# Performance work log

Measured on AMD Instinct MI355X. Metric: run time of the kernel, lower is better.

Reference implementation:

```python
import jax, jax.numpy as jnp
import numpy as np

SINKHORN_ITERS = 4
EPS = 1e-6


def setup_inputs() -> dict:
    key = jax.random.key(0)
    B, T, W, D = 2, 4096, 4, 2048
    k1, k2 = jax.random.split(key, 2)
    x = jax.random.normal(k1, (B, T, W, D), dtype=jnp.float32)
    W_router = jax.random.normal(k2, (W * W + 2 * W, D), dtype=jnp.float32) * 0.02
    b_router = jnp.zeros((W * W + 2 * W,), dtype=jnp.float32)
    return {"x": x, "W_router": W_router, "b_router": b_router}


def _sinkhorn(logits):
    # Bistochastic projection: 4 iterations of alternating row/col normalization.
    def body(w, _):
        w = w / jnp.maximum(w.sum(axis=-1, keepdims=True), EPS)
        w = w / jnp.maximum(w.sum(axis=-2, keepdims=True), EPS)
        return w, None
    w, _ = jax.lax.scan(body, jnp.exp(logits), None, length=SINKHORN_ITERS)
    return w


def reference(x, W_router, b_router):
    B, T, W, D = x.shape
    # router input: mean over the width (stream) dim -> (B, T, D)
    routing_input = x.mean(axis=2)
    raw = routing_input @ W_router.T + b_router          # (B, T, W*W + 2W)
    pre = jax.nn.softmax(raw[..., :W], axis=-1)          # (B, T, W)
    post = jax.nn.softmax(raw[..., W:2 * W], axis=-1)    # (B, T, W)
    res_logits = raw[..., 2 * W:].reshape(B, T, W, W)
    # residual_bias buffer: -2 off-diagonal, +2 on diagonal
    idx = jnp.arange(W)
    bias = jnp.full((W, W), -2.0, dtype=x.dtype).at[idx, idx].set(2.0)
    residual = _sinkhorn(res_logits + bias)              # (B, T, W, W)
    # aggregate streams with pre weights, apply op (identity here)
    aggregated = (x * pre[..., None]).sum(axis=2)        # (B, T, D)
    op_out = aggregated                                  # op = identity
    mixed_residual = jnp.einsum('btij,btjd->btid', residual, x)
    return mixed_residual + post[..., None] * op_out[:, :, None, :]
```

## Files before the change

kernel.cpp:

```cpp
#include <hip/hip_runtime.h>


#define SINKHORN_ITERS 4
#define EPSV 1e-6f

typedef float f32x4 __attribute__((ext_vector_type(4)));

__global__ __launch_bounds__(256, 4) void mchc_fused(
    const float* __restrict__ x,
    const float* __restrict__ Wr,
    const float* __restrict__ br,
    float* __restrict__ out)
{
    const int token = blockIdx.x;
    const int tid   = threadIdx.x;
    const int lane  = tid & 63;
    const int wave  = tid >> 6;

    const f32x4* __restrict__ x4 = (const f32x4*)(x + (size_t)token * 8192);
    const f32x4* __restrict__ w4 = (const f32x4*)Wr;
    f32x4*       __restrict__ o4 = (f32x4*)(out + (size_t)token * 8192);

    f32x4 xa[4], xb[4];
#pragma unroll
    for (int w = 0; w < 4; ++w) {
        xa[w] = __builtin_nontemporal_load(&x4[w * 512 + tid]);
        xb[w] = __builtin_nontemporal_load(&x4[w * 512 + 256 + tid]);
    }

    f32x4 sa = xa[0] + xa[1] + xa[2] + xa[3];
    f32x4 sb = xb[0] + xb[1] + xb[2] + xb[3];

    float p[24];
#pragma unroll
    for (int g = 0; g < 3; ++g) {
        f32x4 wa[8], wb[8];
#pragma unroll
        for (int r = 0; r < 8; ++r) {
            wa[r] = w4[(g * 8 + r) * 512 + tid];
            wb[r] = w4[(g * 8 + r) * 512 + 256 + tid];
        }
        __builtin_amdgcn_sched_barrier(0);
#pragma unroll
        for (int r = 0; r < 8; ++r) {
            f32x4 t = sa * wa[r] + sb * wb[r];
            p[g * 8 + r] = t.x + t.y + t.z + t.w;
        }
    }

    __shared__ float red[4][24];
    __shared__ float rawbuf[24];
    __shared__ float Mbuf[16];

#pragma unroll
    for (int k = 0; k < 24; ++k) {
        float v = p[k];
        v += __shfl_xor(v, 1);
        v += __shfl_xor(v, 2);
        v += __shfl_xor(v, 4);
        v += __shfl_xor(v, 8);
        v += __shfl_xor(v, 16);
        v += __shfl_xor(v, 32);
        p[k] = v;
    }
    if (lane == 0) {
#pragma unroll
        for (int k = 0; k < 24; ++k) red[wave][k] = p[k];
    }
    __syncthreads();

    if (tid < 24) {
        float r = red[0][tid] + red[1][tid] + red[2][tid] + red[3][tid];
        rawbuf[tid] = 0.25f * r + br[tid];
    }
    __syncthreads();

    if (tid < 16) {
        const int i = tid >> 2, j = tid & 3;

        float r0 = rawbuf[0], r1 = rawbuf[1], r2 = rawbuf[2], r3 = rawbuf[3];
        float mp = fmaxf(fmaxf(r0, r1), fmaxf(r2, r3));
        float sp = __expf(r0 - mp) + __expf(r1 - mp) + __expf(r2 - mp) + __expf(r3 - mp);
        float pre_j = __expf(rawbuf[j] - mp) / sp;

        float q0 = rawbuf[4], q1 = rawbuf[5], q2 = rawbuf[6], q3 = rawbuf[7];
        float mq = fmaxf(fmaxf(q0, q1), fmaxf(q2, q3));
        float sq = __expf(q0 - mq) + __expf(q1 - mq) + __expf(q2 - mq) + __expf(q3 - mq);
        float post_i = __expf(rawbuf[4 + i] - mq) / sq;

        float w = __expf(rawbuf[8 + tid] + ((i == j) ? 2.0f : -2.0f));
#pragma unroll
        for (int it = 0; it < SINKHORN_ITERS; ++it) {
            float rs = w + __shfl_xor(w, 1);
            rs += __shfl_xor(rs, 2);
            w /= fmaxf(rs, EPSV);
            float cs = w + __shfl_xor(w, 4);
            cs += __shfl_xor(cs, 8);
            w /= fmaxf(cs, EPSV);
        }
        Mbuf[tid] = w + post_i * pre_j;
    }
    __syncthreads();

    float M[16];
#pragma unroll
    for (int m = 0; m < 16; ++m) M[m] = Mbuf[m];

#pragma unroll
    for (int i = 0; i < 4; ++i) {
        const float m0 = M[i * 4 + 0], m1 = M[i * 4 + 1];
        const float m2 = M[i * 4 + 2], m3 = M[i * 4 + 3];
        f32x4 oa = m0 * xa[0] + m1 * xa[1] + m2 * xa[2] + m3 * xa[3];
        f32x4 ob = m0 * xb[0] + m1 * xb[1] + m2 * xb[2] + m3 * xb[3];
        __builtin_nontemporal_store(oa, &o4[i * 512 + tid]);
        __builtin_nontemporal_store(ob, &o4[i * 512 + 256 + tid]);
    }
}

extern "C" void kernel_launch(void* const* d_in, const int* in_sizes, int n_in,
                              void* d_out, int out_size, void* d_ws, size_t ws_size,
                              hipStream_t stream) {
    const float* x  = (const float*)d_in[0];
    const float* Wr = (const float*)d_in[1];
    const float* br = (const float*)d_in[2];
    float* out = (float*)d_out;

    const int tokens = in_sizes[0] / (4 * 2048);
    mchc_fused<<<dim3(tokens), dim3(256), 0, stream>>>(x, Wr, br, out);
}
```

Before: 601.5 us.

## Map one token per wavefront and remove shared-memory block reductions

Each wavefront now handles one whole token, with four tokens per block, instead of one token per 256-thread block. The router dot products are reduced with a transpose-style butterfly shuffle across lanes. Softmax and Sinkhorn run inside the wave, so the shared-memory buffers and three __syncthreads are gone. The x data is re-read from global memory in the output phase instead of being held in registers, and the nontemporal hints are dropped. This trades lower register pressure and no block barriers for a second read of x, which may hit in cache or may add traffic.

```diff
diff --git a/kernel.cpp b/kernel.cpp
--- a/kernel.cpp
+++ b/kernel.cpp
@@ -12,108 +12,103 @@
     const float* __restrict__ br,
     float* __restrict__ out)
 {
-    const int token = blockIdx.x;
-    const int tid   = threadIdx.x;
-    const int lane  = tid & 63;
-    const int wave  = tid >> 6;
+    const int lane  = threadIdx.x & 63;
+    const int wave  = threadIdx.x >> 6;
+    const int token = blockIdx.x * 4 + wave;
 
     const f32x4* __restrict__ x4 = (const f32x4*)(x + (size_t)token * 8192);
     const f32x4* __restrict__ w4 = (const f32x4*)Wr;
     f32x4*       __restrict__ o4 = (f32x4*)(out + (size_t)token * 8192);
 
-    f32x4 xa[4], xb[4];
+    f32x4 s[8];
 #pragma unroll
-    for (int w = 0; w < 4; ++w) {
-        xa[w] = __builtin_nontemporal_load(&x4[w * 512 + tid]);
-        xb[w] = __builtin_nontemporal_load(&x4[w * 512 + 256 + tid]);
-    }
-
-    f32x4 sa = xa[0] + xa[1] + xa[2] + xa[3];
-    f32x4 sb = xb[0] + xb[1] + xb[2] + xb[3];
+    for (int k = 0; k < 8; ++k) s[k] = x4[k * 64 + lane];
+#pragma unroll
+    for (int w = 1; w < 4; ++w)
+#pragma unroll
+        for (int k = 0; k < 8; ++k) s[k] += x4[w * 512 + k * 64 + lane];
 
     float p[24];
 #pragma unroll
-    for (int g = 0; g < 3; ++g) {
-        f32x4 wa[8], wb[8];
+    for (int r = 0; r < 24; ++r) {
+        f32x4 t = s[0] * w4[r * 512 + lane];
 #pragma unroll
-        for (int r = 0; r < 8; ++r) {
-            wa[r] = w4[(g * 8 + r) * 512 + tid];
-            wb[r] = w4[(g * 8 + r) * 512 + 256 + tid];
-        }
-        __builtin_amdgcn_sched_barrier(0);
+        for (int k = 1; k < 8; ++k)
+            t += s[k] * w4[r * 512 + k * 64 + lane];
+        p[r] = t.x + t.y + t.z + t.w;
+    }
+
+    float raw[8];
 #pragma unroll
-        for (int r = 0; r < 8; ++r) {
-            f32x4 t = sa * wa[r] + sb * wb[r];
-            p[g * 8 + r] = t.x + t.y + t.z + t.w;
+    for (int k = 0; k < 8; ++k) {
+        float v = p[k];
+#pragma unroll
+        for (int d = 1; d < 64; d <<= 1) v += __shfl_xor(v, d);
+        raw[k] = 0.25f * v + br[k];
+    }
+
+    float q[16];
+#pragma unroll
+    for (int m = 0; m < 16; ++m) q[m] = p[8 + m];
+#pragma unroll
+    for (int t = 0; t < 4; ++t) {
+        const int d = 1 << t;
+        const bool hi = (lane & d) != 0;
+#pragma unroll
+        for (int v = 0; v < (8 >> t); ++v) {
+            float a = q[2 * v], b = q[2 * v + 1];
+            float keep = hi ? b : a;
+            float send = hi ? a : b;
+            q[v] = keep + __shfl_xor(send, d);
         }
     }
+    float rsum = q[0];
+    rsum += __shfl_xor(rsum, 16);
+    rsum += __shfl_xor(rsum, 32);
+    const float rw = 0.25f * rsum + br[8 + (lane & 15)];
 
-    __shared__ float red[4][24];
-    __shared__ float rawbuf[24];
-    __shared__ float Mbuf[16];
+    const int i = (lane >> 2) & 3, j = lane & 3;
 
+    float mp = fmaxf(fmaxf(raw[0], raw[1]), fmaxf(raw[2], raw[3]));
+    float e0 = __expf(raw[0] - mp), e1 = __expf(raw[1] - mp);
+    float e2 = __expf(raw[2] - mp), e3 = __expf(raw[3] - mp);
+    float sp = e0 + e1 + e2 + e3;
+    float pre_j = ((j & 1) ? ((j & 2) ? e3 : e1) : ((j & 2) ? e2 : e0)) / sp;
+
+    float mq = fmaxf(fmaxf(raw[4], raw[5]), fmaxf(raw[6], raw[7]));
+    float f0 = __expf(raw[4] - mq), f1 = __expf(raw[5] - mq);
+    float f2 = __expf(raw[6] - mq), f3 = __expf(raw[7] - mq);
+    float sq = f0 + f1 + f2 + f3;
+    float post_i = ((i & 1) ? ((i & 2) ? f3 : f1) : ((i & 2) ? f2 : f0)) / sq;
+
+    float w = __expf(rw + ((i == j) ? 2.0f : -2.0f));
 #pragma unroll
-    for (int k = 0; k < 24; ++k) {
-        float v = p[k];
-        v += __shfl_xor(v, 1);
-        v += __shfl_xor(v, 2);
-        v += __shfl_xor(v, 4);
-        v += __shfl_xor(v, 8);
-        v += __shfl_xor(v, 16);
-        v += __shfl_xor(v, 32);
-        p[k] = v;
+    for (int it = 0; it < SINKHORN_ITERS; ++it) {
+        float rs = w + __shfl_xor(w, 1);
+        rs += __shfl_xor(rs, 2);
+        w /= fmaxf(rs, EPSV);
+        float cs = w + __shfl_xor(w, 4);
+        cs += __shfl_xor(cs, 8);
+        w /= fmaxf(cs, EPSV);
     }
-    if (lane == 0) {
-#pragma unroll
-        for (int k = 0; k < 24; ++k) red[wave][k] = p[k];
-    }
-    __syncthreads();
-
-    if (tid < 24) {
-        float r = red[0][tid] + red[1][tid] + red[2][tid] + red[3][tid];
-        rawbuf[tid] = 0.25f * r + br[tid];
-    }
-    __syncthreads();
-
-    if (tid < 16) {
-        const int i = tid >> 2, j = tid & 3;
-
-        float r0 = rawbuf[0], r1 = rawbuf[1], r2 = rawbuf[2], r3 = rawbuf[3];
-        float mp = fmaxf(fmaxf(r0, r1), fmaxf(r2, r3));
-        float sp = __expf(r0 - mp) + __expf(r1 - mp) + __expf(r2 - mp) + __expf(r3 - mp);
-        float pre_j = __expf(rawbuf[j] - mp) / sp;
-
-        float q0 = rawbuf[4], q1 = rawbuf[5], q2 = rawbuf[6], q3 = rawbuf[7];
-        float mq = fmaxf(fmaxf(q0, q1), fmaxf(q2, q3));
-        float sq = __expf(q0 - mq) + __expf(q1 - mq) + __expf(q2 - mq) + __expf(q3 - mq);
-        float post_i = __expf(rawbuf[4 + i] - mq) / sq;
-
-        float w = __expf(rawbuf[8 + tid] + ((i == j) ? 2.0f : -2.0f));
-#pragma unroll
-        for (int it = 0; it < SINKHORN_ITERS; ++it) {
-            float rs = w + __shfl_xor(w, 1);
-            rs += __shfl_xor(rs, 2);
-            w /= fmaxf(rs, EPSV);
-            float cs = w + __shfl_xor(w, 4);
-            cs += __shfl_xor(cs, 8);
-            w /= fmaxf(cs, EPSV);
-        }
-        Mbuf[tid] = w + post_i * pre_j;
-    }
-    __syncthreads();
+    const float Mval = w + post_i * pre_j;
 
     float M[16];
 #pragma unroll
-    for (int m = 0; m < 16; ++m) M[m] = Mbuf[m];
+    for (int m = 0; m < 16; ++m) M[m] = __shfl(Mval, m);
 
 #pragma unroll
-    for (int i = 0; i < 4; ++i) {
-        const float m0 = M[i * 4 + 0], m1 = M[i * 4 + 1];
-        const float m2 = M[i * 4 + 2], m3 = M[i * 4 + 3];
-        f32x4 oa = m0 * xa[0] + m1 * xa[1] + m2 * xa[2] + m3 * xa[3];
-        f32x4 ob = m0 * xb[0] + m1 * xb[1] + m2 * xb[2] + m3 * xb[3];
-        __builtin_nontemporal_store(oa, &o4[i * 512 + tid]);
-        __builtin_nontemporal_store(ob, &o4[i * 512 + 256 + tid]);
+    for (int k = 0; k < 8; ++k) {
+        f32x4 x0 = x4[0 * 512 + k * 64 + lane];
+        f32x4 x1 = x4[1 * 512 + k * 64 + lane];
+        f32x4 x2 = x4[2 * 512 + k * 64 + lane];
+        f32x4 x3 = x4[3 * 512 + k * 64 + lane];
+#pragma unroll
+        for (int r = 0; r < 4; ++r) {
+            f32x4 o = M[r * 4 + 0] * x0 + M[r * 4 + 1] * x1
+                    + M[r * 4 + 2] * x2 + M[r * 4 + 3] * x3;
+            o4[r * 512 + k * 64 + lane] = o;
+        }
     }
 }
 
@@ -126,5 +121,5 @@
     float* out = (float*)d_out;
 
     const int tokens = in_sizes[0] / (4 * 2048);
-    mchc_fused<<<dim3(tokens), dim3(256), 0, stream>>>(x, Wr, br, out);
+    mchc_fused<<<dim3(tokens / 4), dim3(256), 0, stream>>>(x, Wr, br, out);
 }
```

Measured after the change: 580.4 us. -3.5%, faster.
